# Performance work log

Hardware: AMD Instinct MI355X
Metric: run time of the kernel (lower is better)

## Reference

```python
import jax, jax.numpy as jnp
import numpy as np
from jax import lax

T, B, E = 128, 32, 4096
H = 512            # hidden per direction
K = 20             # tagset size
START, STOP = 18, 19
NEG = -10000.0


def setup_inputs() -> dict:
    key = jax.random.key(0)
    ks = jax.random.split(key, 12)
    s = 0.02
    x = jax.random.normal(ks[0], (T, B, E), dtype=jnp.float32)
    tags = jax.random.randint(ks[1], (B, T), 0, 18)  # gold tags, exclude START/STOP
    W_e2n = jax.random.normal(ks[2], (E, E), dtype=jnp.float32) * s
    b_e2n = jnp.zeros((E,), jnp.float32)
    # LSTM params, torch gate order (i, f, g, o); biases b_ih + b_hh fused
    W_ih_f = jax.random.normal(ks[3], (4 * H, E), dtype=jnp.float32) * s
    W_hh_f = jax.random.normal(ks[4], (4 * H, H), dtype=jnp.float32) * s
    b_f = jnp.zeros((4 * H,), jnp.float32)
    W_ih_b = jax.random.normal(ks[5], (4 * H, E), dtype=jnp.float32) * s
    W_hh_b = jax.random.normal(ks[6], (4 * H, H), dtype=jnp.float32) * s
    b_b = jnp.zeros((4 * H,), jnp.float32)
    W_lin = jax.random.normal(ks[7], (K, 2 * H), dtype=jnp.float32) * s
    b_lin = jnp.zeros((K,), jnp.float32)
    trans = jax.random.normal(ks[8], (K, K), dtype=jnp.float32)
    trans = trans.at[START, :].set(NEG).at[:, STOP].set(NEG)
    return dict(x=x, tags=tags, W_e2n=W_e2n, b_e2n=b_e2n,
                W_ih_f=W_ih_f, W_hh_f=W_hh_f, b_f=b_f,
                W_ih_b=W_ih_b, W_hh_b=W_hh_b, b_b=b_b,
                W_lin=W_lin, b_lin=b_lin, trans=trans)


def _lstm_dir(x, W_ih, W_hh, b, reverse):
    # x: [T, B, E] -> hidden states [T, B, H]
    xg = jnp.einsum('tbe,ge->tbg', x, W_ih) + b  # [T, B, 4H]
    if reverse:
        xg = xg[::-1]
    h0 = jnp.zeros((x.shape[1], W_hh.shape[1]), x.dtype)

    def step(carry, g_x):
        h, c = carry
        g = g_x + h @ W_hh.T
        i, f, gg, o = jnp.split(g, 4, axis=-1)
        i = jax.nn.sigmoid(i); f = jax.nn.sigmoid(f)
        gg = jnp.tanh(gg); o = jax.nn.sigmoid(o)
        c = f * c + i * gg
        h = o * jnp.tanh(c)
        return (h, c), h

    _, hs = lax.scan(step, (h0, h0), xg)
    return hs[::-1] if reverse else hs


def _features(x, W_e2n, b_e2n, W_ih_f, W_hh_f, b_f, W_ih_b, W_hh_b, b_b, W_lin, b_lin):
    # embedding2nn (relearn_embeddings)
    x = jnp.einsum('tbe,fe->tbf', x, W_e2n) + b_e2n
    hf = _lstm_dir(x, W_ih_f, W_hh_f, b_f, reverse=False)
    hb = _lstm_dir(x, W_ih_b, W_hh_b, b_b, reverse=True)
    h = jnp.concatenate([hf, hb], axis=-1)            # [T, B, 2H]
    feats = jnp.einsum('tbh,kh->tbk', h, W_lin) + b_lin  # [T, B, K]
    return jnp.swapaxes(feats, 0, 1)                  # [B, T, K]


def _crf_nll(feats, tags, trans):
    # feats [B, T, K]; trans[i, j] = score(j -> i)
    Bn, Tn, Kn = feats.shape
    alpha0 = jnp.full((Bn, Kn), NEG, feats.dtype).at[:, START].set(0.0)

    def step(alpha, emit):
        # alpha[b, prev] + trans[next, prev], logsumexp over prev, + emission
        scores = alpha[:, None, :] + trans[None, :, :]     # [B, next, prev]
        return jax.nn.logsumexp(scores, axis=2) + emit, None

    alpha, _ = lax.scan(step, alpha0, jnp.swapaxes(feats, 0, 1))
    log_Z = jax.nn.logsumexp(alpha + trans[STOP][None, :], axis=1)  # [B]

    # gold path score
    prev = jnp.concatenate([jnp.full((Bn, 1), START, tags.dtype), tags], axis=1)
    nxt = jnp.concatenate([tags, jnp.full((Bn, 1), STOP, tags.dtype)], axis=1)
    trans_score = trans[nxt, prev].sum(axis=1)
    emit_score = jnp.take_along_axis(feats, tags[:, :, None], axis=2)[..., 0].sum(axis=1)
    return log_Z - (trans_score + emit_score)  # [B]


def reference(x, tags, W_e2n, b_e2n, W_ih_f, W_hh_f, b_f,
              W_ih_b, W_hh_b, b_b, W_lin, b_lin, trans):
    feats = _features(x, W_e2n, b_e2n, W_ih_f, W_hh_f, b_f,
                      W_ih_b, W_hh_b, b_b, W_lin, b_lin)
    return _crf_nll(feats, tags, trans)
```

## Files before the change

kernel.cpp:

```cpp
#include <hip/hip_runtime.h>
#include <stdint.h>


#define NEGV (-10000.0f)

typedef __bf16          bf16x8 __attribute__((ext_vector_type(8)));
typedef float           f32x4  __attribute__((ext_vector_type(4)));
typedef unsigned short  u16x8  __attribute__((ext_vector_type(8)));

typedef const __attribute__((address_space(1))) unsigned int* as1p;
typedef __attribute__((address_space(3))) unsigned int* as3p;

__device__ __forceinline__ void lds_cp16(const void* g, void* l) {
  __builtin_amdgcn_global_load_lds((as1p)g, (as3p)l, 16, 0, 0);
}

__device__ __forceinline__ unsigned short f2bf(float f) {
  unsigned int u = __float_as_uint(f);
  u += 0x7fffu + ((u >> 16) & 1u);
  return (unsigned short)(u >> 16);
}
__device__ __forceinline__ float bf2f(unsigned short h) {
  return __uint_as_float(((unsigned int)h) << 16);
}

__global__ __launch_bounds__(256) void cvt_f32_bf16(const float* __restrict__ in,
                                                    unsigned short* __restrict__ out,
                                                    int n4) {
  int stride = gridDim.x * blockDim.x;
  for (int i = blockIdx.x * blockDim.x + threadIdx.x; i < n4; i += stride) {
    float4 f = ((const float4*)in)[i];
    ushort4 o;
    o.x = f2bf(f.x); o.y = f2bf(f.y); o.z = f2bf(f.z); o.w = f2bf(f.w);
    ((ushort4*)out)[i] = o;
  }
}

__global__ __launch_bounds__(256) void gemm_bf16(const unsigned short* __restrict__ A,
                                                 const unsigned short* __restrict__ B,
                                                 unsigned short* __restrict__ C,
                                                 const float* __restrict__ bias0,
                                                 const float* __restrict__ bias1,
                                                 int nsplit, int M, int N, int K) {
  __shared__ unsigned short As[128 * 32];
  __shared__ unsigned short Bs[128 * 32];
  const int tid   = threadIdx.x;
  const int lane  = tid & 63;
  const int wm    = (tid >> 6) >> 1;
  const int wn    = (tid >> 6) & 1;
  const int nb    = N >> 7;
  const int bm    = (int)(blockIdx.x / nb) << 7;
  const int bn    = (int)(blockIdx.x % nb) << 7;
  const int srow  = tid >> 2;
  const int skoff = (tid & 3) * 8;
  const int lrow  = lane & 15;
  const int lk    = (lane >> 4) * 8;

  f32x4 acc[4][4];
#pragma unroll
  for (int i = 0; i < 4; ++i)
#pragma unroll
    for (int j = 0; j < 4; ++j) acc[i][j] = (f32x4){0.f, 0.f, 0.f, 0.f};

  for (int k0 = 0; k0 < K; k0 += 32) {
    lds_cp16(A + (size_t)(bm + srow) * K + k0 + skoff,      &As[tid * 8]);
    lds_cp16(A + (size_t)(bm + 64 + srow) * K + k0 + skoff, &As[2048 + tid * 8]);
    lds_cp16(B + (size_t)(bn + srow) * K + k0 + skoff,      &Bs[tid * 8]);
    lds_cp16(B + (size_t)(bn + 64 + srow) * K + k0 + skoff, &Bs[2048 + tid * 8]);
    __syncthreads();
    bf16x8 af[4], bfr[4];
#pragma unroll
    for (int mi = 0; mi < 4; ++mi)
      af[mi] = *(const bf16x8*)&As[(wm * 64 + mi * 16 + lrow) * 32 + lk];
#pragma unroll
    for (int ni = 0; ni < 4; ++ni)
      bfr[ni] = *(const bf16x8*)&Bs[(wn * 64 + ni * 16 + lrow) * 32 + lk];
#pragma unroll
    for (int mi = 0; mi < 4; ++mi)
#pragma unroll
      for (int ni = 0; ni < 4; ++ni)
        acc[mi][ni] = __builtin_amdgcn_mfma_f32_16x16x32_bf16(af[mi], bfr[ni], acc[mi][ni], 0, 0, 0);
    __syncthreads();
  }

#pragma unroll
  for (int mi = 0; mi < 4; ++mi) {
#pragma unroll
    for (int ni = 0; ni < 4; ++ni) {
      const int col = bn + wn * 64 + ni * 16 + lrow;
      const float bv = (col < nsplit) ? bias0[col] : bias1[col - nsplit];
#pragma unroll
      for (int j = 0; j < 4; ++j) {
        const int row = bm + wm * 64 + mi * 16 + (lane >> 4) * 4 + j;
        C[(size_t)row * N + col] = f2bf(acc[mi][ni][j] + bv);
      }
    }
  }
}

__global__ __launch_bounds__(256) void lstm_step(const unsigned short* __restrict__ Whh,
                                                 const unsigned short* __restrict__ xg,
                                                 unsigned short* __restrict__ hstate,
                                                 float* __restrict__ cstate,
                                                 unsigned short* __restrict__ hseq,
                                                 int s) {
  const int dir  = blockIdx.x >> 4;
  const int cg   = blockIdx.x & 15;
  const int t    = dir ? (127 - s) : s;
  const int lane = threadIdx.x & 63;
  const int wid  = threadIdx.x >> 6;
  const int mh   = wid & 1;
  const int ch   = wid >> 1;
  const int colbase = cg * 32 + ch * 16;
  const int lrow = lane & 15;
  const int lk   = (lane >> 4) * 8;

  const unsigned short* hprev = hstate + (size_t)(((s & 1) * 2 + dir) * 32) * 512;
  u16x8 afr[16];
#pragma unroll
  for (int kk = 0; kk < 16; ++kk)
    afr[kk] = *(const u16x8*)&hprev[(mh * 16 + lrow) * 512 + kk * 32 + lk];

  f32x4 acc[4];
#pragma unroll
  for (int g = 0; g < 4; ++g) acc[g] = (f32x4){0.f, 0.f, 0.f, 0.f};

#pragma unroll
  for (int g = 0; g < 4; ++g) {
    const unsigned short* wp = Whh + (size_t)(dir * 2048 + g * 512 + colbase + lrow) * 512 + lk;
#pragma unroll
    for (int kk = 0; kk < 16; ++kk) {
      u16x8 bq = *(const u16x8*)&wp[kk * 32];
      acc[g] = __builtin_amdgcn_mfma_f32_16x16x32_bf16(
          __builtin_bit_cast(bf16x8, afr[kk]), __builtin_bit_cast(bf16x8, bq), acc[g], 0, 0, 0);
    }
  }

  unsigned short* hnext = hstate + (size_t)((((s + 1) & 1) * 2 + dir) * 32) * 512;
  float* cst = cstate + (size_t)dir * 32 * 512;
  const int col = colbase + lrow;
#pragma unroll
  for (int j = 0; j < 4; ++j) {
    const int b = mh * 16 + (lane >> 4) * 4 + j;
    const size_t xrow = (size_t)(t * 32 + b) * 4096 + dir * 2048;
    float vi = acc[0][j] + bf2f(xg[xrow + 0 * 512 + col]);
    float vf = acc[1][j] + bf2f(xg[xrow + 1 * 512 + col]);
    float vg = acc[2][j] + bf2f(xg[xrow + 2 * 512 + col]);
    float vo = acc[3][j] + bf2f(xg[xrow + 3 * 512 + col]);
    float ig = 1.f / (1.f + expf(-vi));
    float fg = 1.f / (1.f + expf(-vf));
    float gv = tanhf(vg);
    float og = 1.f / (1.f + expf(-vo));
    float cn = fg * cst[b * 512 + col] + ig * gv;
    cst[b * 512 + col] = cn;
    float hv = og * tanhf(cn);
    unsigned short hb = f2bf(hv);
    hnext[b * 512 + col] = hb;
    hseq[(size_t)(t * 32 + b) * 1024 + dir * 512 + col] = hb;
  }
}

__global__ __launch_bounds__(256) void feats_gemv(const unsigned short* __restrict__ hseq,
                                                  const float* __restrict__ Wlin,
                                                  const float* __restrict__ blin,
                                                  float* __restrict__ feats) {
  const int lane = threadIdx.x & 63;
  const int wid  = threadIdx.x >> 6;
  const int row  = blockIdx.x * 4 + wid;
  const int t = row >> 5, b = row & 31;
  const unsigned short* hr = hseq + (size_t)row * 1024 + lane * 16;
  float hf[16];
  u16x8 h0 = *(const u16x8*)hr;
  u16x8 h1 = *(const u16x8*)(hr + 8);
#pragma unroll
  for (int i = 0; i < 8; ++i) { hf[i] = bf2f(h0[i]); hf[8 + i] = bf2f(h1[i]); }
  for (int k = 0; k < 20; ++k) {
    const float* wr = Wlin + k * 1024 + lane * 16;
    float p = 0.f;
#pragma unroll
    for (int q = 0; q < 4; ++q) {
      float4 w4 = ((const float4*)wr)[q];
      p += hf[q*4+0]*w4.x + hf[q*4+1]*w4.y + hf[q*4+2]*w4.z + hf[q*4+3]*w4.w;
    }
#pragma unroll
    for (int off = 32; off; off >>= 1) p += __shfl_xor(p, off);
    if (lane == 0) feats[(size_t)b * (128 * 20) + t * 20 + k] = p + blin[k];
  }
}

__global__ __launch_bounds__(64) void crf_nll(const float* __restrict__ feats,
                                              const int* __restrict__ tags,
                                              const float* __restrict__ trans,
                                              float* __restrict__ out) {
  const int b = blockIdx.x;
  const int j = threadIdx.x;
  const bool act = j < 20;
  float tr[20];
#pragma unroll
  for (int p = 0; p < 20; ++p) tr[p] = act ? trans[j * 20 + p] : 0.f;
  float alpha = (j == 18) ? 0.f : NEGV;
  const float* fb = feats + (size_t)b * (128 * 20);
  for (int t = 0; t < 128; ++t) {
    float emit = act ? fb[t * 20 + j] : 0.f;
    float sc[20];
    float m = -1e30f;
#pragma unroll
    for (int p = 0; p < 20; ++p) {
      float ap = __shfl(alpha, p);
      sc[p] = ap + tr[p];
      m = fmaxf(m, sc[p]);
    }
    float sum = 0.f;
#pragma unroll
    for (int p = 0; p < 20; ++p) sum += expf(sc[p] - m);
    alpha = m + logf(sum) + emit;
  }
  float v = act ? (alpha + trans[19 * 20 + j]) : -1e30f;
  float m2 = v;
#pragma unroll
  for (int off = 32; off; off >>= 1) m2 = fmaxf(m2, __shfl_xor(m2, off));
  float s2 = expf(v - m2);
#pragma unroll
  for (int off = 32; off; off >>= 1) s2 += __shfl_xor(s2, off);
  const float logZ = m2 + logf(s2);

  const int* tg = tags + b * 128;
  float ts;
  {
    int prev = (j == 0) ? 18 : tg[j - 1];
    ts = trans[tg[j] * 20 + prev];
    ts += trans[tg[j + 64] * 20 + tg[j + 63]];
    if (j == 0) ts += trans[19 * 20 + tg[127]];
  }
  float es = fb[j * 20 + tg[j]] + fb[(j + 64) * 20 + tg[j + 64]];
  float tot = ts + es;
#pragma unroll
  for (int off = 32; off; off >>= 1) tot += __shfl_xor(tot, off);
  if (j == 0) out[b] = logZ - tot;
}

extern "C" void kernel_launch(void* const* d_in, const int* in_sizes, int n_in,
                              void* d_out, int out_size, void* d_ws, size_t ws_size,
                              hipStream_t stream) {
  const float* x     = (const float*)d_in[0];
  const int*   tags  = (const int*)d_in[1];
  const float* We2n  = (const float*)d_in[2];
  const float* be2n  = (const float*)d_in[3];
  const float* Wihf  = (const float*)d_in[4];
  const float* Whhf  = (const float*)d_in[5];
  const float* bf_   = (const float*)d_in[6];
  const float* Wihb  = (const float*)d_in[7];
  const float* Whhb  = (const float*)d_in[8];
  const float* bb_   = (const float*)d_in[9];
  const float* Wlin  = (const float*)d_in[10];
  const float* blin  = (const float*)d_in[11];
  const float* trans = (const float*)d_in[12];

  char* ws = (char*)d_ws;
  unsigned short* buf0   = (unsigned short*)(ws);
  unsigned short* buf1   = (unsigned short*)(ws + 33554432ULL);
  unsigned short* buf2   = (unsigned short*)(ws + 2ULL * 33554432ULL);
  unsigned short* whhb   = (unsigned short*)(ws + 3ULL * 33554432ULL);
  unsigned short* hseq   = (unsigned short*)(ws + 3ULL * 33554432ULL + 4194304ULL);
  unsigned short* hstate = (unsigned short*)(ws + 3ULL * 33554432ULL + 12582912ULL);
  float*          cstate = (float*)(ws + 3ULL * 33554432ULL + 12713984ULL);
  float*          feats  = (float*)(ws + 3ULL * 33554432ULL + 12845056ULL);

  cvt_f32_bf16<<<2048, 256, 0, stream>>>(x,    buf0, 16777216 / 4);
  cvt_f32_bf16<<<2048, 256, 0, stream>>>(We2n, buf1, 16777216 / 4);
  cvt_f32_bf16<<<512,  256, 0, stream>>>(Whhf, whhb,            1048576 / 4);
  cvt_f32_bf16<<<512,  256, 0, stream>>>(Whhb, whhb + 1048576,  1048576 / 4);
  hipMemsetAsync(hstate, 0, 262144, stream);

  gemm_bf16<<<1024, 256, 0, stream>>>(buf0, buf1, buf2, be2n, be2n, 4096, 4096, 4096, 4096);

  cvt_f32_bf16<<<2048, 256, 0, stream>>>(Wihf, buf1,           8388608 / 4);
  cvt_f32_bf16<<<2048, 256, 0, stream>>>(Wihb, buf1 + 8388608, 8388608 / 4);

  gemm_bf16<<<1024, 256, 0, stream>>>(buf2, buf1, buf0, bf_, bb_, 2048, 4096, 4096, 4096);

  for (int s = 0; s < 128; ++s)
    lstm_step<<<32, 256, 0, stream>>>(whhb, buf0, hstate, cstate, hseq, s);

  feats_gemv<<<1024, 256, 0, stream>>>(hseq, Wlin, blin, feats);

  crf_nll<<<32, 64, 0, stream>>>(feats, tags, trans, (float*)d_out);
}
```

Baseline: 2.444 ms.

## Replace per-step LSTM launches with persistent cooperative kernel using grid sync

The 128 separate lstm_step launches are replaced by a single cooperative persistent kernel. Each block keeps its slice of W_hh resident in LDS, holds the cell state in registers, and uses grid.sync between time steps. Gate results pass through shared memory so each thread applies the nonlinearities for fixed (batch, column) pairs. This removes per-step launch overhead and the repeated global reloads of W_hh and c. The cost is grid-wide barriers, about 160KB of LDS per block, and a dependence on cooperative launch support. The hstate memset is also shrunk to cover only the initial buffer.

```diff
diff --git a/kernel.cpp b/kernel.cpp
--- a/kernel.cpp
+++ b/kernel.cpp
@@ -1,8 +1,11 @@
 #include <hip/hip_runtime.h>
+#include <hip/hip_cooperative_groups.h>
 #include <stdint.h>
 
 
 #define NEGV (-10000.0f)
+
+namespace cg = cooperative_groups;
 
 typedef __bf16          bf16x8 __attribute__((ext_vector_type(8)));
 typedef float           f32x4  __attribute__((ext_vector_type(4)));
@@ -98,65 +101,106 @@
   }
 }
 
-__global__ __launch_bounds__(256) void lstm_step(const unsigned short* __restrict__ Whh,
-                                                 const unsigned short* __restrict__ xg,
-                                                 unsigned short* __restrict__ hstate,
-                                                 float* __restrict__ cstate,
-                                                 unsigned short* __restrict__ hseq,
-                                                 int s) {
-  const int dir  = blockIdx.x >> 4;
-  const int cg   = blockIdx.x & 15;
-  const int t    = dir ? (127 - s) : s;
-  const int lane = threadIdx.x & 63;
-  const int wid  = threadIdx.x >> 6;
-  const int mh   = wid & 1;
-  const int ch   = wid >> 1;
-  const int colbase = cg * 32 + ch * 16;
+__global__ __launch_bounds__(512) void lstm_persist(const unsigned short* __restrict__ Whh,
+                                                    const unsigned short* __restrict__ xg,
+                                                    unsigned short* __restrict__ hstate,
+                                                    unsigned short* __restrict__ hseq) {
+  __shared__ unsigned short Wlds[4 * 32 * 520];
+  __shared__ float G[4 * 32 * 36];
+
+  cg::grid_group grid = cg::this_grid();
+
+  const int bid  = blockIdx.x;
+  const int dir  = bid >> 4;
+  const int cgc  = bid & 15;
+  const int colbase = cgc * 32;
+  const int tid  = threadIdx.x;
+  const int lane = tid & 63;
+  const int wid  = tid >> 6;
+  const int g    = wid & 3;
+  const int mh   = wid >> 2;
   const int lrow = lane & 15;
-  const int lk   = (lane >> 4) * 8;
-
-  const unsigned short* hprev = hstate + (size_t)(((s & 1) * 2 + dir) * 32) * 512;
-  u16x8 afr[16];
-#pragma unroll
-  for (int kk = 0; kk < 16; ++kk)
-    afr[kk] = *(const u16x8*)&hprev[(mh * 16 + lrow) * 512 + kk * 32 + lk];
-
-  f32x4 acc[4];
-#pragma unroll
-  for (int g = 0; g < 4; ++g) acc[g] = (f32x4){0.f, 0.f, 0.f, 0.f};
-
-#pragma unroll
-  for (int g = 0; g < 4; ++g) {
-    const unsigned short* wp = Whh + (size_t)(dir * 2048 + g * 512 + colbase + lrow) * 512 + lk;
-#pragma unroll
-    for (int kk = 0; kk < 16; ++kk) {
-      u16x8 bq = *(const u16x8*)&wp[kk * 32];
-      acc[g] = __builtin_amdgcn_mfma_f32_16x16x32_bf16(
-          __builtin_bit_cast(bf16x8, afr[kk]), __builtin_bit_cast(bf16x8, bq), acc[g], 0, 0, 0);
-    }
-  }
-
-  unsigned short* hnext = hstate + (size_t)((((s + 1) & 1) * 2 + dir) * 32) * 512;
-  float* cst = cstate + (size_t)dir * 32 * 512;
-  const int col = colbase + lrow;
-#pragma unroll
-  for (int j = 0; j < 4; ++j) {
-    const int b = mh * 16 + (lane >> 4) * 4 + j;
-    const size_t xrow = (size_t)(t * 32 + b) * 4096 + dir * 2048;
-    float vi = acc[0][j] + bf2f(xg[xrow + 0 * 512 + col]);
-    float vf = acc[1][j] + bf2f(xg[xrow + 1 * 512 + col]);
-    float vg = acc[2][j] + bf2f(xg[xrow + 2 * 512 + col]);
-    float vo = acc[3][j] + bf2f(xg[xrow + 3 * 512 + col]);
-    float ig = 1.f / (1.f + expf(-vi));
-    float fg = 1.f / (1.f + expf(-vf));
-    float gv = tanhf(vg);
-    float og = 1.f / (1.f + expf(-vo));
-    float cn = fg * cst[b * 512 + col] + ig * gv;
-    cst[b * 512 + col] = cn;
-    float hv = og * tanhf(cn);
-    unsigned short hb = f2bf(hv);
-    hnext[b * 512 + col] = hb;
-    hseq[(size_t)(t * 32 + b) * 1024 + dir * 512 + col] = hb;
+  const int lk4  = lane >> 4;
+  const int lk   = lk4 * 8;
+
+  for (int idx = tid; idx < 4 * 32 * 64; idx += 512) {
+    const int g2 = idx >> 11;
+    const int r  = (idx >> 6) & 31;
+    const int c  = idx & 63;
+    u16x8 v = *(const u16x8*)&Whh[(size_t)(dir * 2048 + g2 * 512 + colbase + r) * 512 + c * 8];
+    *(u16x8*)&Wlds[(g2 * 32 + r) * 520 + c * 8] = v;
+  }
+  __syncthreads();
+
+  const int b0  = tid >> 5,        col0 = tid & 31;
+  const int b1  = (tid + 512) >> 5, col1 = tid & 31;
+  float creg0 = 0.f, creg1 = 0.f;
+
+  for (int s = 0; s < 128; ++s) {
+    const int t = dir ? (127 - s) : s;
+
+    unsigned short xv0[4], xv1[4];
+    {
+      const size_t xr0 = (size_t)(t * 32 + b0) * 4096 + dir * 2048 + colbase + col0;
+      const size_t xr1 = (size_t)(t * 32 + b1) * 4096 + dir * 2048 + colbase + col1;
+#pragma unroll
+      for (int g2 = 0; g2 < 4; ++g2) { xv0[g2] = xg[xr0 + g2 * 512]; xv1[g2] = xg[xr1 + g2 * 512]; }
+    }
+
+    const unsigned short* hp = hstate + (size_t)((s & 1) * 2 + dir) * 32 * 512;
+    u16x8 a[16];
+#pragma unroll
+    for (int kk = 0; kk < 16; ++kk)
+      a[kk] = *(const u16x8*)&hp[(mh * 16 + lrow) * 512 + kk * 32 + lk];
+
+    f32x4 acc[2] = {(f32x4){0.f,0.f,0.f,0.f}, (f32x4){0.f,0.f,0.f,0.f}};
+#pragma unroll
+    for (int ct = 0; ct < 2; ++ct)
+#pragma unroll
+      for (int kk = 0; kk < 16; ++kk) {
+        u16x8 w = *(const u16x8*)&Wlds[(g * 32 + ct * 16 + lrow) * 520 + kk * 32 + lk];
+        acc[ct] = __builtin_amdgcn_mfma_f32_16x16x32_bf16(
+            __builtin_bit_cast(bf16x8, a[kk]), __builtin_bit_cast(bf16x8, w), acc[ct], 0, 0, 0);
+      }
+
+#pragma unroll
+    for (int ct = 0; ct < 2; ++ct)
+#pragma unroll
+      for (int j = 0; j < 4; ++j)
+        G[g * 1152 + (mh * 16 + lk4 * 4 + j) * 36 + ct * 16 + lrow] = acc[ct][j];
+    __syncthreads();
+
+    unsigned short* hn = hstate + (size_t)(((s + 1) & 1) * 2 + dir) * 32 * 512;
+    {
+      float vi = G[0 * 1152 + b0 * 36 + col0] + bf2f(xv0[0]);
+      float vf = G[1 * 1152 + b0 * 36 + col0] + bf2f(xv0[1]);
+      float vg = G[2 * 1152 + b0 * 36 + col0] + bf2f(xv0[2]);
+      float vo = G[3 * 1152 + b0 * 36 + col0] + bf2f(xv0[3]);
+      float ig = 1.f / (1.f + expf(-vi));
+      float fg = 1.f / (1.f + expf(-vf));
+      float gv = tanhf(vg);
+      float og = 1.f / (1.f + expf(-vo));
+      creg0 = fg * creg0 + ig * gv;
+      unsigned short hb = f2bf(og * tanhf(creg0));
+      hn[b0 * 512 + colbase + col0] = hb;
+      hseq[(size_t)(t * 32 + b0) * 1024 + dir * 512 + colbase + col0] = hb;
+    }
+    {
+      float vi = G[0 * 1152 + b1 * 36 + col1] + bf2f(xv1[0]);
+      float vf = G[1 * 1152 + b1 * 36 + col1] + bf2f(xv1[1]);
+      float vg = G[2 * 1152 + b1 * 36 + col1] + bf2f(xv1[2]);
+      float vo = G[3 * 1152 + b1 * 36 + col1] + bf2f(xv1[3]);
+      float ig = 1.f / (1.f + expf(-vi));
+      float fg = 1.f / (1.f + expf(-vf));
+      float gv = tanhf(vg);
+      float og = 1.f / (1.f + expf(-vo));
+      creg1 = fg * creg1 + ig * gv;
+      unsigned short hb = f2bf(og * tanhf(creg1));
+      hn[b1 * 512 + colbase + col1] = hb;
+      hseq[(size_t)(t * 32 + b1) * 1024 + dir * 512 + colbase + col1] = hb;
+    }
+
+    grid.sync();
   }
 }
 
@@ -263,14 +307,13 @@
   unsigned short* whhb   = (unsigned short*)(ws + 3ULL * 33554432ULL);
   unsigned short* hseq   = (unsigned short*)(ws + 3ULL * 33554432ULL + 4194304ULL);
   unsigned short* hstate = (unsigned short*)(ws + 3ULL * 33554432ULL + 12582912ULL);
-  float*          cstate = (float*)(ws + 3ULL * 33554432ULL + 12713984ULL);
   float*          feats  = (float*)(ws + 3ULL * 33554432ULL + 12845056ULL);
 
   cvt_f32_bf16<<<2048, 256, 0, stream>>>(x,    buf0, 16777216 / 4);
   cvt_f32_bf16<<<2048, 256, 0, stream>>>(We2n, buf1, 16777216 / 4);
   cvt_f32_bf16<<<512,  256, 0, stream>>>(Whhf, whhb,            1048576 / 4);
   cvt_f32_bf16<<<512,  256, 0, stream>>>(Whhb, whhb + 1048576,  1048576 / 4);
-  hipMemsetAsync(hstate, 0, 262144, stream);
+  hipMemsetAsync(hstate, 0, 131072, stream);
 
   gemm_bf16<<<1024, 256, 0, stream>>>(buf0, buf1, buf2, be2n, be2n, 4096, 4096, 4096, 4096);
 
@@ -279,8 +322,10 @@
 
   gemm_bf16<<<1024, 256, 0, stream>>>(buf2, buf1, buf0, bf_, bb_, 2048, 4096, 4096, 4096);
 
-  for (int s = 0; s < 128; ++s)
-    lstm_step<<<32, 256, 0, stream>>>(whhb, buf0, hstate, cstate, hseq, s);
+  {
+    void* args[] = { (void*)&whhb, (void*)&buf0, (void*)&hstate, (void*)&hseq };
+    hipLaunchCooperativeKernel((void*)lstm_persist, dim3(32), dim3(512), args, 0, stream);
+  }
 
   feats_gemv<<<1024, 256, 0, stream>>>(hseq, Wlin, blin, feats);
 
```

Measured after the change: 2.188 ms. 10.5% less time.
